# Kernel tuning notes

Measured on AMD Instinct MI355X. Metric: run time of the kernel, lower is better.

## Reference

```python
import jax, jax.numpy as jnp
import numpy as np

N_NODES = 100000
N_EDGES = 3200000
IN_CH = 128
HID_CH = 128   # 2 * out_channels
OUT_CH = 64


def setup_inputs() -> dict:
    key = jax.random.key(0)
    ks = jax.random.split(key, 6)
    x = jax.random.normal(ks[0], (N_NODES, IN_CH), dtype=jnp.float32)
    edge_index = jax.random.randint(ks[1], (2, N_EDGES), 0, N_NODES, dtype=jnp.int64)
    # Glorot-ish init for GCN linear weights
    W1 = jax.random.normal(ks[2], (IN_CH, HID_CH), dtype=jnp.float32) / np.sqrt(IN_CH)
    b1 = jnp.zeros((HID_CH,), dtype=jnp.float32)
    W2 = jax.random.normal(ks[3], (HID_CH, OUT_CH), dtype=jnp.float32) / np.sqrt(HID_CH)
    b2 = jnp.zeros((OUT_CH,), dtype=jnp.float32)
    return {"x": x, "edge_index": edge_index, "W1": W1, "b1": b1, "W2": W2, "b2": b2}


def gcn_conv(x, src, dst, W, b, n):
    """PyG GCNConv: add self-loops, symmetric D^-1/2 (A+I) D^-1/2 normalization,
    linear transform, scatter-add aggregation, then bias."""
    h = x @ W  # [N, C_out]
    ones = jnp.ones(src.shape[0], dtype=x.dtype)
    deg = jax.ops.segment_sum(ones, dst, num_segments=n) + 1.0  # self-loop degree
    dinv = jax.lax.rsqrt(deg)  # [N]
    coef = dinv[src] * dinv[dst]  # [E] edge normalization
    agg = jax.ops.segment_sum(h[src] * coef[:, None], dst, num_segments=n)
    agg = agg + h * (dinv * dinv)[:, None]  # self-loop contribution
    return agg + b


def reference(x, edge_index, W1, b1, W2, b2):
    src, dst = edge_index[0], edge_index[1]
    n = x.shape[0]
    h = jax.nn.relu(gcn_conv(x, src, dst, W1, b1, n))
    out = jax.nn.relu(gcn_conv(h, src, dst, W2, b2, n))
    return out
```

## Files before the change

kernel.cpp:

```cpp
#include <hip/hip_runtime.h>
#include <hip/hip_fp16.h>
#include <cstdint>
#include <cstddef>


#define BSHIFT 8
#define CAP    12288

typedef _Float16 half8 __attribute__((ext_vector_type(8)));
typedef float f32x4 __attribute__((ext_vector_type(4)));

__global__ __launch_bounds__(256) void k_binit(int* __restrict__ bktcur, int nbkt) {
  int b = blockIdx.x * 256 + threadIdx.x;
  if (b < nbkt) bktcur[b] = b * CAP;
}

__global__ __launch_bounds__(256) void k_part(const int* __restrict__ src,
                                              const int* __restrict__ dst,
                                              int* __restrict__ bktcur,
                                              int* __restrict__ part, int E,
                                              int nbkt) {
  __shared__ int hist[512];
  const int tid = threadIdx.x;
  const int e0 = blockIdx.x * 4096;
  for (int b = tid; b < nbkt; b += 256) hist[b] = 0;
  __syncthreads();
#pragma unroll
  for (int j = 0; j < 16; ++j) {
    const int e = e0 + j * 256 + tid;
    if (e < E) atomicAdd(&hist[dst[e] >> BSHIFT], 1);
  }
  __syncthreads();
  for (int b = tid; b < nbkt; b += 256) {
    const int c = hist[b];
    hist[b] = c ? atomicAdd(&bktcur[b], c) : 0;
  }
  __syncthreads();
#pragma unroll
  for (int j = 0; j < 16; ++j) {
    const int e = e0 + j * 256 + tid;
    if (e < E) {
      const int d = dst[e];
      const int bkt = d >> BSHIFT;
      const int pos = atomicAdd(&hist[bkt], 1);
      if (pos < (bkt + 1) * CAP)
        part[pos] = (src[e] << BSHIFT) | (d & ((1 << BSHIFT) - 1));
    }
  }
}

__global__ __launch_bounds__(256) void k_bktscan(const int* __restrict__ bktcur,
                                                 int* __restrict__ bktbase,
                                                 int* __restrict__ offsets, int n,
                                                 int E, int nbkt) {
  __shared__ int sc[512];
  const int t = threadIdx.x;
  sc[t] = (t < nbkt) ? (bktcur[t] - t * CAP) : 0;
  sc[256 + t] = (256 + t < nbkt) ? (bktcur[256 + t] - (256 + t) * CAP) : 0;
  __syncthreads();
  if (t == 0) {
    int run = 0;
    for (int b = 0; b < nbkt; ++b) {
      const int c = sc[b];
      sc[b] = run;
      run += c;
    }
    offsets[n] = E;
    bktbase[nbkt] = E;
  }
  __syncthreads();
  if (t < nbkt) bktbase[t] = sc[t];
  if (256 + t < nbkt) bktbase[256 + t] = sc[256 + t];
}

__global__ __launch_bounds__(256) void k_csr2(const int* __restrict__ part,
                                              const int* __restrict__ bktcur,
                                              const int* __restrict__ bktbase,
                                              int* __restrict__ offsets,
                                              int* __restrict__ csr_src,
                                              float* __restrict__ dinv, int n) {
  __shared__ int cnt[256];
  __shared__ int ts[256];
  const int b = blockIdx.x;
  const int node0 = b << BSHIFT;
  const int nn = min(256, n - node0);
  const int t = threadIdx.x;
  cnt[t] = 0;
  __syncthreads();
  const int w0p = b * CAP;
  const int w1p = min(bktcur[b], w0p + CAP);
  for (int e = w0p + t; e < w1p; e += 256)
    atomicAdd(&cnt[part[e] & ((1 << BSHIFT) - 1)], 1);
  __syncthreads();
  const int c = cnt[t];
  ts[t] = c;
  __syncthreads();
  for (int off = 1; off < 256; off <<= 1) {
    const int u = (t >= off) ? ts[t - off] : 0;
    __syncthreads();
    ts[t] += u;
    __syncthreads();
  }
  const int excl = ts[t] - c;
  const int w0 = bktbase[b];
  if (t < nn) {
    offsets[node0 + t] = w0 + excl;
    dinv[node0 + t] = rsqrtf((float)c + 1.0f);
  }
  cnt[t] = w0 + excl;
  __syncthreads();
  for (int e = w0p + t; e < w1p; e += 256) {
    const int p = part[e];
    const int pos = atomicAdd(&cnt[p & ((1 << BSHIFT) - 1)], 1);
    csr_src[pos] = p >> BSHIFT;
  }
}

template <typename TA, int COLS>
__global__ __launch_bounds__(256) void k_gemm_mfma(const TA* __restrict__ A,
                                                   const float* __restrict__ W,
                                                   const float* __restrict__ dinv,
                                                   __half* __restrict__ Hout,
                                                   int N, int ntiles) {
  constexpr int RW = (COLS == 128) ? 2 : 4;
  constexpr int RPT = RW * 16;
  __shared__ _Float16 Wt[128 * COLS];
  __shared__ _Float16 Lb[4][16][72];
  const int tid = threadIdx.x;
  const int w = tid >> 6;
  const int l = tid & 63;

  for (int f = tid; f < (128 * COLS) / 4; f += 256) {
    const int k = f / (COLS / 4);
    const int c4 = (f % (COLS / 4)) * 4;
    const float4 wv = *reinterpret_cast<const float4*>(W + (size_t)k * COLS + c4);
#pragma unroll
    for (int j = 0; j < 4; ++j) {
      const int cc = c4 + j;
      Wt[(cc * 128 + k) ^ ((cc & 7) << 3)] = (_Float16)(&wv.x)[j];
    }
  }
  __syncthreads();

  const int colw = (COLS == 128) ? (w >> 1) * 64 : 0;
  const int rw = (COLS == 128) ? (w & 1) : w;
  const int koff = (l >> 4) * 8;

  half8 bf[4][4];
#pragma unroll
  for (int t = 0; t < 4; ++t)
#pragma unroll
    for (int s = 0; s < 4; ++s) {
      const int cc = colw + 16 * t + (l & 15);
      const int kk = 32 * s + koff;
      bf[t][s] =
          *reinterpret_cast<const half8*>(&Wt[(cc * 128 + kk) ^ ((cc & 7) << 3)]);
    }

  for (int tile = blockIdx.x; tile < ntiles; tile += gridDim.x) {
    const int row = tile * RPT + rw * 16 + (l & 15);
    const int rowc = (row < N) ? row : (N - 1);
    f32x4 acc[4];
#pragma unroll
    for (int t = 0; t < 4; ++t) acc[t] = (f32x4){0.f, 0.f, 0.f, 0.f};

#pragma unroll
    for (int s = 0; s < 4; ++s) {
      half8 af;
      if constexpr (sizeof(TA) == 4) {
        const float* ap = (const float*)A + (size_t)rowc * 128 + 32 * s + koff;
        const float4 a0 = *reinterpret_cast<const float4*>(ap);
        const float4 a1 = *reinterpret_cast<const float4*>(ap + 4);
#pragma unroll
        for (int j = 0; j < 4; ++j) {
          af[j] = (_Float16)(&a0.x)[j];
          af[4 + j] = (_Float16)(&a1.x)[j];
        }
      } else {
        af = *reinterpret_cast<const half8*>((const __half*)A +
                                             (size_t)rowc * 128 + 32 * s + koff);
      }
#pragma unroll
      for (int t = 0; t < 4; ++t)
        acc[t] = __builtin_amdgcn_mfma_f32_16x16x32_f16(af, bf[t][s], acc[t],
                                                        0, 0, 0);
    }

    const int rbase = tile * RPT + rw * 16 + (l >> 4) * 4;
    float dr[4];
#pragma unroll
    for (int r = 0; r < 4; ++r) {
      const int rr = rbase + r;
      dr[r] = (rr < N) ? dinv[rr] : 0.f;
    }

#pragma unroll
    for (int t = 0; t < 4; ++t)
#pragma unroll
      for (int r = 0; r < 4; ++r)
        Lb[w][(l >> 4) * 4 + r][16 * t + (l & 15)] = (_Float16)(acc[t][r] * dr[r]);
    const int orow = tile * RPT + rw * 16 + (l & 15);
    if (orow < N) {
      const int ch = (l >> 4) * 16;
      const half8 v0 = *reinterpret_cast<const half8*>(&Lb[w][l & 15][ch]);
      const half8 v1 = *reinterpret_cast<const half8*>(&Lb[w][l & 15][ch + 8]);
      __half* hp = Hout + (size_t)orow * COLS + colw + ch;
      *reinterpret_cast<half8*>(hp) = v0;
      *reinterpret_cast<half8*>(hp + 8) = v1;
    }
  }
}

__global__ __launch_bounds__(256) void k_gather128(
    const __half* __restrict__ H, const int* __restrict__ offsets,
    const int* __restrict__ csr_src, const float* __restrict__ dinv,
    const float* __restrict__ bias, __half* __restrict__ out, int N) {
  const int lane = threadIdx.x & 63;
  const int g = lane >> 3;
  const int sl = lane & 7;
  int w = (blockIdx.x * 256 + threadIdx.x) >> 6;
  const int nw = (gridDim.x * 256) >> 6;
  for (int i = w; i < N; i += nw) {
    const int beg = offsets[i];
    const int end = offsets[i + 1];
    float acc[16];
    {
      const float vf = (g == 0) ? 1.f : 0.f;
      const float4 ha = *reinterpret_cast<const float4*>(H + (size_t)i * 128 + sl * 16);
      const float4 hb = *reinterpret_cast<const float4*>(H + (size_t)i * 128 + sl * 16 + 8);
      const __half2* pa = reinterpret_cast<const __half2*>(&ha);
      const __half2* pb = reinterpret_cast<const __half2*>(&hb);
#pragma unroll
      for (int q = 0; q < 4; ++q) {
        const float2 fa = __half22float2(pa[q]);
        const float2 fb = __half22float2(pb[q]);
        acc[q * 2] = vf * fa.x;
        acc[q * 2 + 1] = vf * fa.y;
        acc[8 + q * 2] = vf * fb.x;
        acc[8 + q * 2 + 1] = vf * fb.y;
      }
    }
    int base = beg;
    for (; base + 16 <= end; base += 16) {
      const int s0 = __builtin_nontemporal_load(csr_src + base + g);
      const int s1 = __builtin_nontemporal_load(csr_src + base + 8 + g);
      const float4 h0a = *reinterpret_cast<const float4*>(H + (size_t)s0 * 128 + sl * 16);
      const float4 h0b = *reinterpret_cast<const float4*>(H + (size_t)s0 * 128 + sl * 16 + 8);
      const float4 h1a = *reinterpret_cast<const float4*>(H + (size_t)s1 * 128 + sl * 16);
      const float4 h1b = *reinterpret_cast<const float4*>(H + (size_t)s1 * 128 + sl * 16 + 8);
      const __half2* p0a = reinterpret_cast<const __half2*>(&h0a);
      const __half2* p0b = reinterpret_cast<const __half2*>(&h0b);
      const __half2* p1a = reinterpret_cast<const __half2*>(&h1a);
      const __half2* p1b = reinterpret_cast<const __half2*>(&h1b);
#pragma unroll
      for (int q = 0; q < 4; ++q) {
        const float2 f0a = __half22float2(p0a[q]);
        const float2 f0b = __half22float2(p0b[q]);
        const float2 f1a = __half22float2(p1a[q]);
        const float2 f1b = __half22float2(p1b[q]);
        acc[q * 2] += f0a.x + f1a.x;
        acc[q * 2 + 1] += f0a.y + f1a.y;
        acc[8 + q * 2] += f0b.x + f1b.x;
        acc[8 + q * 2 + 1] += f0b.y + f1b.y;
      }
    }
    for (; base < end; base += 8) {
      const int e = base + g;
      const bool v = e < end;
      const int s = v ? __builtin_nontemporal_load(csr_src + e) : i;
      const float vf = v ? 1.f : 0.f;
      const float4 ha = *reinterpret_cast<const float4*>(H + (size_t)s * 128 + sl * 16);
      const float4 hb = *reinterpret_cast<const float4*>(H + (size_t)s * 128 + sl * 16 + 8);
      const __half2* pa = reinterpret_cast<const __half2*>(&ha);
      const __half2* pb = reinterpret_cast<const __half2*>(&hb);
#pragma unroll
      for (int q = 0; q < 4; ++q) {
        const float2 fa = __half22float2(pa[q]);
        const float2 fb = __half22float2(pb[q]);
        acc[q * 2] = fmaf(vf, fa.x, acc[q * 2]);
        acc[q * 2 + 1] = fmaf(vf, fa.y, acc[q * 2 + 1]);
        acc[8 + q * 2] = fmaf(vf, fb.x, acc[8 + q * 2]);
        acc[8 + q * 2 + 1] = fmaf(vf, fb.y, acc[8 + q * 2 + 1]);
      }
    }
#pragma unroll
    for (int j = 0; j < 16; ++j) {
      float a = acc[j];
      a += __shfl_xor(a, 8);
      a += __shfl_xor(a, 16);
      a += __shfl_xor(a, 32);
      acc[j] = a;
    }
    if (g == 0) {
      const float di = dinv[i];
      __half2 ov[8];
#pragma unroll
      for (int q = 0; q < 8; ++q) {
        const float2 bv = *reinterpret_cast<const float2*>(bias + sl * 16 + q * 2);
        ov[q] = __floats2half2_rn(fmaxf(fmaf(di, acc[q * 2], bv.x), 0.f),
                                  fmaxf(fmaf(di, acc[q * 2 + 1], bv.y), 0.f));
      }
      __half* op = out + (size_t)i * 128 + sl * 16;
      *reinterpret_cast<float4*>(op) = *reinterpret_cast<const float4*>(&ov[0]);
      *reinterpret_cast<float4*>(op + 8) = *reinterpret_cast<const float4*>(&ov[4]);
    }
  }
}

__global__ __launch_bounds__(256) void k_gather64(
    const __half* __restrict__ H, const int* __restrict__ offsets,
    const int* __restrict__ csr_src, const float* __restrict__ dinv,
    const float* __restrict__ bias, float* __restrict__ out, int N) {
  const int lane = threadIdx.x & 63;
  const int g = lane >> 3;
  const int sl = lane & 7;
  int w = (blockIdx.x * 256 + threadIdx.x) >> 6;
  const int nw = (gridDim.x * 256) >> 6;
  for (int i = w; i < N; i += nw) {
    const int beg = offsets[i];
    const int end = offsets[i + 1];
    float acc[8];
    {
      const float vf = (g == 0) ? 1.f : 0.f;
      const float4 ha = *reinterpret_cast<const float4*>(H + (size_t)i * 64 + sl * 8);
      const __half2* pa = reinterpret_cast<const __half2*>(&ha);
#pragma unroll
      for (int q = 0; q < 4; ++q) {
        const float2 fa = __half22float2(pa[q]);
        acc[q * 2] = vf * fa.x;
        acc[q * 2 + 1] = vf * fa.y;
      }
    }
    int base = beg;
    for (; base + 16 <= end; base += 16) {
      const int s0 = __builtin_nontemporal_load(csr_src + base + g);
      const int s1 = __builtin_nontemporal_load(csr_src + base + 8 + g);
      const float4 h0 = *reinterpret_cast<const float4*>(H + (size_t)s0 * 64 + sl * 8);
      const float4 h1 = *reinterpret_cast<const float4*>(H + (size_t)s1 * 64 + sl * 8);
      const __half2* p0 = reinterpret_cast<const __half2*>(&h0);
      const __half2* p1 = reinterpret_cast<const __half2*>(&h1);
#pragma unroll
      for (int q = 0; q < 4; ++q) {
        const float2 f0 = __half22float2(p0[q]);
        const float2 f1 = __half22float2(p1[q]);
        acc[q * 2] += f0.x + f1.x;
        acc[q * 2 + 1] += f0.y + f1.y;
      }
    }
    for (; base < end; base += 8) {
      const int e = base + g;
      const bool v = e < end;
      const int s = v ? __builtin_nontemporal_load(csr_src + e) : i;
      const float vf = v ? 1.f : 0.f;
      const float4 ha = *reinterpret_cast<const float4*>(H + (size_t)s * 64 + sl * 8);
      const __half2* pa = reinterpret_cast<const __half2*>(&ha);
#pragma unroll
      for (int q = 0; q < 4; ++q) {
        const float2 fa = __half22float2(pa[q]);
        acc[q * 2] = fmaf(vf, fa.x, acc[q * 2]);
        acc[q * 2 + 1] = fmaf(vf, fa.y, acc[q * 2 + 1]);
      }
    }
#pragma unroll
    for (int j = 0; j < 8; ++j) {
      float a = acc[j];
      a += __shfl_xor(a, 8);
      a += __shfl_xor(a, 16);
      a += __shfl_xor(a, 32);
      acc[j] = a;
    }
    if (g == 0) {
      const float di = dinv[i];
      float* op = out + (size_t)i * 64 + sl * 8;
      const float4 b0 = *reinterpret_cast<const float4*>(bias + sl * 8);
      const float4 b1 = *reinterpret_cast<const float4*>(bias + sl * 8 + 4);
      float4 o;
      o.x = fmaxf(fmaf(di, acc[0], b0.x), 0.f);
      o.y = fmaxf(fmaf(di, acc[1], b0.y), 0.f);
      o.z = fmaxf(fmaf(di, acc[2], b0.z), 0.f);
      o.w = fmaxf(fmaf(di, acc[3], b0.w), 0.f);
      *reinterpret_cast<float4*>(op) = o;
      o.x = fmaxf(fmaf(di, acc[4], b1.x), 0.f);
      o.y = fmaxf(fmaf(di, acc[5], b1.y), 0.f);
      o.z = fmaxf(fmaf(di, acc[6], b1.z), 0.f);
      o.w = fmaxf(fmaf(di, acc[7], b1.w), 0.f);
      *reinterpret_cast<float4*>(op + 4) = o;
    }
  }
}

extern "C" void kernel_launch(void* const* d_in, const int* in_sizes, int n_in,
                              void* d_out, int out_size, void* d_ws,
                              size_t ws_size, hipStream_t stream) {
  const float* x  = (const float*)d_in[0];
  const int*   ei = (const int*)d_in[1];
  const float* W1 = (const float*)d_in[2];
  const float* b1 = (const float*)d_in[3];
  const float* W2 = (const float*)d_in[4];
  const float* b2 = (const float*)d_in[5];

  const int IN  = 128;
  const int n   = in_sizes[0] / IN;
  const int E   = in_sizes[1] / 2;
  const int* srcv = ei;
  const int* dstv = ei + E;
  float* out = (float*)d_out;

  const int NBKT = (n + 255) >> BSHIFT;
  const int NCHK = (E + 4095) / 4096;
  const int NT1  = (n + 31) / 32;
  const int NT2  = (n + 63) / 64;

  char* p = (char*)d_ws;
  auto take = [&](size_t bytes) {
    char* r = p;
    p += (bytes + 255) & ~(size_t)255;
    return r;
  };
  float*  dinv    = (float*)take((size_t)n * 4);
  int*    offsets = (int*)take((size_t)(n + 1) * 4);
  int*    bktbase = (int*)take(512 * 4);
  int*    bktcur  = (int*)take(512 * 4);
  int*    csr_src = (int*)take((size_t)E * 4);
  __half* H16     = (__half*)take((size_t)n * 128 * 2);
  __half* hprime  = (__half*)take((size_t)n * 128 * 2);
  int*    part    = (int*)hprime;

  k_binit<<<(NBKT + 255) / 256, 256, 0, stream>>>(bktcur, NBKT);
  k_part<<<NCHK, 256, 0, stream>>>(srcv, dstv, bktcur, part, E, NBKT);
  k_bktscan<<<1, 256, 0, stream>>>(bktcur, bktbase, offsets, n, E, NBKT);
  k_csr2<<<NBKT, 256, 0, stream>>>(part, bktcur, bktbase, offsets, csr_src,
                                   dinv, n);

  k_gemm_mfma<float, 128><<<512, 256, 0, stream>>>(x, W1, dinv, H16, n, NT1);
  k_gather128<<<25000, 256, 0, stream>>>(H16, offsets, csr_src, dinv, b1,
                                         hprime, n);

  k_gemm_mfma<__half, 64><<<512, 256, 0, stream>>>(hprime, W2, dinv, H16, n, NT2);
  k_gather64<<<25000, 256, 0, stream>>>(H16, offsets, csr_src, dinv, b2,
                                        out, n);
}
```

Baseline: 316.0 us.

## Two-pass radix partition by source then destination; shrink gather grid

Edges are first bucketed by source node, then re-bucketed by destination in a second pass. Because the second pass is stable, each destination bucket comes out with its edges in roughly sorted source order, so later neighbor gathers read features with better locality. This adds a full extra pass over the edge list, plus a scratch buffer aliased onto H16. The gather kernels also drop from 25000 to 2048 blocks, which assumes they loop over nodes with a grid stride.

```diff
diff --git a/kernel.cpp b/kernel.cpp
--- a/kernel.cpp
+++ b/kernel.cpp
@@ -10,16 +10,20 @@
 typedef _Float16 half8 __attribute__((ext_vector_type(8)));
 typedef float f32x4 __attribute__((ext_vector_type(4)));
 
-__global__ __launch_bounds__(256) void k_binit(int* __restrict__ bktcur, int nbkt) {
+__global__ __launch_bounds__(256) void k_binit2(int* __restrict__ cur0,
+                                                int* __restrict__ cur1, int nbkt) {
   int b = blockIdx.x * 256 + threadIdx.x;
-  if (b < nbkt) bktcur[b] = b * CAP;
-}
-
-__global__ __launch_bounds__(256) void k_part(const int* __restrict__ src,
-                                              const int* __restrict__ dst,
-                                              int* __restrict__ bktcur,
-                                              int* __restrict__ part, int E,
-                                              int nbkt) {
+  if (b < nbkt) {
+    cur0[b] = b * CAP;
+    cur1[b] = b * CAP;
+  }
+}
+
+__global__ __launch_bounds__(256) void k_part0(const int* __restrict__ src,
+                                               const int* __restrict__ dst,
+                                               int* __restrict__ cur0,
+                                               int* __restrict__ part0, int E,
+                                               int nbkt) {
   __shared__ int hist[512];
   const int tid = threadIdx.x;
   const int e0 = blockIdx.x * 4096;
@@ -28,7 +32,52 @@
 #pragma unroll
   for (int j = 0; j < 16; ++j) {
     const int e = e0 + j * 256 + tid;
-    if (e < E) atomicAdd(&hist[dst[e] >> BSHIFT], 1);
+    if (e < E) atomicAdd(&hist[src[e] >> BSHIFT], 1);
+  }
+  __syncthreads();
+  for (int b = tid; b < nbkt; b += 256) {
+    const int c = hist[b];
+    hist[b] = c ? atomicAdd(&cur0[b], c) : 0;
+  }
+  __syncthreads();
+#pragma unroll
+  for (int j = 0; j < 16; ++j) {
+    const int e = e0 + j * 256 + tid;
+    if (e < E) {
+      const int s = src[e];
+      const int bkt = s >> BSHIFT;
+      const int pos = atomicAdd(&hist[bkt], 1);
+      if (pos < (bkt + 1) * CAP)
+        part0[pos] = (dst[e] << BSHIFT) | (s & ((1 << BSHIFT) - 1));
+    }
+  }
+}
+
+__global__ __launch_bounds__(256) void k_part1(const int* __restrict__ part0,
+                                               const int* __restrict__ cur0,
+                                               int* __restrict__ bktcur,
+                                               int* __restrict__ part, int nbkt) {
+  __shared__ int hist[512];
+  const int tid = threadIdx.x;
+  const int e0 = blockIdx.x * 4096;
+  for (int b = tid; b < nbkt; b += 256) hist[b] = 0;
+  __syncthreads();
+  int fv[16];
+  int db[16];
+#pragma unroll
+  for (int j = 0; j < 16; ++j) {
+    const int pos = e0 + j * 256 + tid;
+    const int sb = pos / CAP;
+    db[j] = -1;
+    fv[j] = 0;
+    if (sb < nbkt && pos < cur0[sb]) {
+      const int p = __builtin_nontemporal_load(part0 + pos);
+      const int d = p >> BSHIFT;
+      const int s = (sb << BSHIFT) | (p & ((1 << BSHIFT) - 1));
+      fv[j] = (s << BSHIFT) | (d & ((1 << BSHIFT) - 1));
+      db[j] = d >> BSHIFT;
+      atomicAdd(&hist[db[j]], 1);
+    }
   }
   __syncthreads();
   for (int b = tid; b < nbkt; b += 256) {
@@ -38,13 +87,9 @@
   __syncthreads();
 #pragma unroll
   for (int j = 0; j < 16; ++j) {
-    const int e = e0 + j * 256 + tid;
-    if (e < E) {
-      const int d = dst[e];
-      const int bkt = d >> BSHIFT;
-      const int pos = atomicAdd(&hist[bkt], 1);
-      if (pos < (bkt + 1) * CAP)
-        part[pos] = (src[e] << BSHIFT) | (d & ((1 << BSHIFT) - 1));
+    if (db[j] >= 0) {
+      const int pos = atomicAdd(&hist[db[j]], 1);
+      if (pos < (db[j] + 1) * CAP) part[pos] = fv[j];
     }
   }
 }
@@ -408,6 +453,7 @@
 
   const int NBKT = (n + 255) >> BSHIFT;
   const int NCHK = (E + 4095) / 4096;
+  const int NP1  = (NBKT * CAP + 4095) / 4096;
   const int NT1  = (n + 31) / 32;
   const int NT2  = (n + 63) / 64;
 
@@ -421,22 +467,25 @@
   int*    offsets = (int*)take((size_t)(n + 1) * 4);
   int*    bktbase = (int*)take(512 * 4);
   int*    bktcur  = (int*)take(512 * 4);
+  int*    bktcur0 = (int*)take(512 * 4);
   int*    csr_src = (int*)take((size_t)E * 4);
   __half* H16     = (__half*)take((size_t)n * 128 * 2);
   __half* hprime  = (__half*)take((size_t)n * 128 * 2);
+  int*    part0   = (int*)H16;
   int*    part    = (int*)hprime;
 
-  k_binit<<<(NBKT + 255) / 256, 256, 0, stream>>>(bktcur, NBKT);
-  k_part<<<NCHK, 256, 0, stream>>>(srcv, dstv, bktcur, part, E, NBKT);
+  k_binit2<<<(NBKT + 255) / 256, 256, 0, stream>>>(bktcur0, bktcur, NBKT);
+  k_part0<<<NCHK, 256, 0, stream>>>(srcv, dstv, bktcur0, part0, E, NBKT);
+  k_part1<<<NP1, 256, 0, stream>>>(part0, bktcur0, bktcur, part, NBKT);
   k_bktscan<<<1, 256, 0, stream>>>(bktcur, bktbase, offsets, n, E, NBKT);
   k_csr2<<<NBKT, 256, 0, stream>>>(part, bktcur, bktbase, offsets, csr_src,
                                    dinv, n);
 
   k_gemm_mfma<float, 128><<<512, 256, 0, stream>>>(x, W1, dinv, H16, n, NT1);
-  k_gather128<<<25000, 256, 0, stream>>>(H16, offsets, csr_src, dinv, b1,
-                                         hprime, n);
+  k_gather128<<<2048, 256, 0, stream>>>(H16, offsets, csr_src, dinv, b1,
+                                        hprime, n);
 
   k_gemm_mfma<__half, 64><<<512, 256, 0, stream>>>(hprime, W2, dinv, H16, n, NT2);
-  k_gather64<<<25000, 256, 0, stream>>>(H16, offsets, csr_src, dinv, b2,
-                                        out, n);
-}
+  k_gather64<<<2048, 256, 0, stream>>>(H16, offsets, csr_src, dinv, b2,
+                                       out, n);
+}
```

Measured after the change: 355.7 us. 1.13x slower.

## Split layer-1 features into two 64-column halves for cache-friendlier gathers

Applied to the files above, without the earlier changes.

Stores the first GEMM output as two separate 64-column fp16 arrays and aggregates each half with its own gather pass, reusing the 64-wide gather kernel templated on fp16/fp32 output. The second GEMM reads its input from the two halves. The intent is to halve the random-access working set per gather pass so neighbour rows hit cache more often, at the cost of reading the CSR structure twice and an extra launch.

```diff
diff --git a/kernel.cpp b/kernel.cpp
--- a/kernel.cpp
+++ b/kernel.cpp
@@ -116,14 +116,14 @@
   }
 }
 
-template <typename TA, int COLS>
-__global__ __launch_bounds__(256) void k_gemm_mfma(const TA* __restrict__ A,
-                                                   const float* __restrict__ W,
-                                                   const float* __restrict__ dinv,
-                                                   __half* __restrict__ Hout,
-                                                   int N, int ntiles) {
-  constexpr int RW = (COLS == 128) ? 2 : 4;
-  constexpr int RPT = RW * 16;
+__global__ __launch_bounds__(256) void k_gemm1(const float* __restrict__ A,
+                                               const float* __restrict__ W,
+                                               const float* __restrict__ dinv,
+                                               __half* __restrict__ Hlo,
+                                               __half* __restrict__ Hhi,
+                                               int N, int ntiles) {
+  constexpr int COLS = 128;
+  constexpr int RPT = 32;
   __shared__ _Float16 Wt[128 * COLS];
   __shared__ _Float16 Lb[4][16][72];
   const int tid = threadIdx.x;
@@ -142,8 +142,8 @@
   }
   __syncthreads();
 
-  const int colw = (COLS == 128) ? (w >> 1) * 64 : 0;
-  const int rw = (COLS == 128) ? (w & 1) : w;
+  const int colw = (w >> 1) * 64;
+  const int rw = w & 1;
   const int koff = (l >> 4) * 8;
 
   half8 bf[4][4];
@@ -167,18 +167,13 @@
 #pragma unroll
     for (int s = 0; s < 4; ++s) {
       half8 af;
-      if constexpr (sizeof(TA) == 4) {
-        const float* ap = (const float*)A + (size_t)rowc * 128 + 32 * s + koff;
-        const float4 a0 = *reinterpret_cast<const float4*>(ap);
-        const float4 a1 = *reinterpret_cast<const float4*>(ap + 4);
-#pragma unroll
-        for (int j = 0; j < 4; ++j) {
-          af[j] = (_Float16)(&a0.x)[j];
-          af[4 + j] = (_Float16)(&a1.x)[j];
-        }
-      } else {
-        af = *reinterpret_cast<const half8*>((const __half*)A +
-                                             (size_t)rowc * 128 + 32 * s + koff);
+      const float* ap = A + (size_t)rowc * 128 + 32 * s + koff;
+      const float4 a0 = *reinterpret_cast<const float4*>(ap);
+      const float4 a1 = *reinterpret_cast<const float4*>(ap + 4);
+#pragma unroll
+      for (int j = 0; j < 4; ++j) {
+        af[j] = (_Float16)(&a0.x)[j];
+        af[4 + j] = (_Float16)(&a1.x)[j];
       }
 #pragma unroll
       for (int t = 0; t < 4; ++t)
@@ -204,113 +199,103 @@
       const int ch = (l >> 4) * 16;
       const half8 v0 = *reinterpret_cast<const half8*>(&Lb[w][l & 15][ch]);
       const half8 v1 = *reinterpret_cast<const half8*>(&Lb[w][l & 15][ch + 8]);
-      __half* hp = Hout + (size_t)orow * COLS + colw + ch;
+      __half* base = (colw == 0) ? Hlo : Hhi;
+      __half* hp = base + (size_t)orow * 64 + ch;
       *reinterpret_cast<half8*>(hp) = v0;
       *reinterpret_cast<half8*>(hp + 8) = v1;
     }
   }
 }
 
-__global__ __launch_bounds__(256) void k_gather128(
+__global__ __launch_bounds__(256) void k_gemm2(const __half* __restrict__ Alo,
+                                               const __half* __restrict__ Ahi,
+                                               const float* __restrict__ W,
+                                               const float* __restrict__ dinv,
+                                               __half* __restrict__ Hout,
+                                               int N, int ntiles) {
+  constexpr int COLS = 64;
+  constexpr int RPT = 64;
+  __shared__ _Float16 Wt[128 * COLS];
+  __shared__ _Float16 Lb[4][16][72];
+  const int tid = threadIdx.x;
+  const int w = tid >> 6;
+  const int l = tid & 63;
+
+  for (int f = tid; f < (128 * COLS) / 4; f += 256) {
+    const int k = f / (COLS / 4);
+    const int c4 = (f % (COLS / 4)) * 4;
+    const float4 wv = *reinterpret_cast<const float4*>(W + (size_t)k * COLS + c4);
+#pragma unroll
+    for (int j = 0; j < 4; ++j) {
+      const int cc = c4 + j;
+      Wt[(cc * 128 + k) ^ ((cc & 7) << 3)] = (_Float16)(&wv.x)[j];
+    }
+  }
+  __syncthreads();
+
+  const int rw = w;
+  const int koff = (l >> 4) * 8;
+
+  half8 bf[4][4];
+#pragma unroll
+  for (int t = 0; t < 4; ++t)
+#pragma unroll
+    for (int s = 0; s < 4; ++s) {
+      const int cc = 16 * t + (l & 15);
+      const int kk = 32 * s + koff;
+      bf[t][s] =
+          *reinterpret_cast<const half8*>(&Wt[(cc * 128 + kk) ^ ((cc & 7) << 3)]);
+    }
+
+  for (int tile = blockIdx.x; tile < ntiles; tile += gridDim.x) {
+    const int row = tile * RPT + rw * 16 + (l & 15);
+    const int rowc = (row < N) ? row : (N - 1);
+    f32x4 acc[4];
+#pragma unroll
+    for (int t = 0; t < 4; ++t) acc[t] = (f32x4){0.f, 0.f, 0.f, 0.f};
+
+#pragma unroll
+    for (int s = 0; s < 4; ++s) {
+      const __half* ab = (s < 2) ? Alo : Ahi;
+      const int kk = (s & 1) * 32 + koff;
+      const half8 af =
+          *reinterpret_cast<const half8*>(ab + (size_t)rowc * 64 + kk);
+#pragma unroll
+      for (int t = 0; t < 4; ++t)
+        acc[t] = __builtin_amdgcn_mfma_f32_16x16x32_f16(af, bf[t][s], acc[t],
+                                                        0, 0, 0);
+    }
+
+    const int rbase = tile * RPT + rw * 16 + (l >> 4) * 4;
+    float dr[4];
+#pragma unroll
+    for (int r = 0; r < 4; ++r) {
+      const int rr = rbase + r;
+      dr[r] = (rr < N) ? dinv[rr] : 0.f;
+    }
+
+#pragma unroll
+    for (int t = 0; t < 4; ++t)
+#pragma unroll
+      for (int r = 0; r < 4; ++r)
+        Lb[w][(l >> 4) * 4 + r][16 * t + (l & 15)] = (_Float16)(acc[t][r] * dr[r]);
+    const int orow = tile * RPT + rw * 16 + (l & 15);
+    if (orow < N) {
+      const int ch = (l >> 4) * 16;
+      const half8 v0 = *reinterpret_cast<const half8*>(&Lb[w][l & 15][ch]);
+      const half8 v1 = *reinterpret_cast<const half8*>(&Lb[w][l & 15][ch + 8]);
+      __half* hp = Hout + (size_t)orow * 64 + ch;
+      *reinterpret_cast<half8*>(hp) = v0;
+      *reinterpret_cast<half8*>(hp + 8) = v1;
+    }
+  }
+}
+
+template <int OUT16>
+__global__ __launch_bounds__(256) void k_gather64t(
     const __half* __restrict__ H, const int* __restrict__ offsets,
     const int* __restrict__ csr_src, const float* __restrict__ dinv,
-    const float* __restrict__ bias, __half* __restrict__ out, int N) {
-  const int lane = threadIdx.x & 63;
-  const int g = lane >> 3;
-  const int sl = lane & 7;
-  int w = (blockIdx.x * 256 + threadIdx.x) >> 6;
-  const int nw = (gridDim.x * 256) >> 6;
-  for (int i = w; i < N; i += nw) {
-    const int beg = offsets[i];
-    const int end = offsets[i + 1];
-    float acc[16];
-    {
-      const float vf = (g == 0) ? 1.f : 0.f;
-      const float4 ha = *reinterpret_cast<const float4*>(H + (size_t)i * 128 + sl * 16);
-      const float4 hb = *reinterpret_cast<const float4*>(H + (size_t)i * 128 + sl * 16 + 8);
-      const __half2* pa = reinterpret_cast<const __half2*>(&ha);
-      const __half2* pb = reinterpret_cast<const __half2*>(&hb);
-#pragma unroll
-      for (int q = 0; q < 4; ++q) {
-        const float2 fa = __half22float2(pa[q]);
-        const float2 fb = __half22float2(pb[q]);
-        acc[q * 2] = vf * fa.x;
-        acc[q * 2 + 1] = vf * fa.y;
-        acc[8 + q * 2] = vf * fb.x;
-        acc[8 + q * 2 + 1] = vf * fb.y;
-      }
-    }
-    int base = beg;
-    for (; base + 16 <= end; base += 16) {
-      const int s0 = __builtin_nontemporal_load(csr_src + base + g);
-      const int s1 = __builtin_nontemporal_load(csr_src + base + 8 + g);
-      const float4 h0a = *reinterpret_cast<const float4*>(H + (size_t)s0 * 128 + sl * 16);
-      const float4 h0b = *reinterpret_cast<const float4*>(H + (size_t)s0 * 128 + sl * 16 + 8);
-      const float4 h1a = *reinterpret_cast<const float4*>(H + (size_t)s1 * 128 + sl * 16);
-      const float4 h1b = *reinterpret_cast<const float4*>(H + (size_t)s1 * 128 + sl * 16 + 8);
-      const __half2* p0a = reinterpret_cast<const __half2*>(&h0a);
-      const __half2* p0b = reinterpret_cast<const __half2*>(&h0b);
-      const __half2* p1a = reinterpret_cast<const __half2*>(&h1a);
-      const __half2* p1b = reinterpret_cast<const __half2*>(&h1b);
-#pragma unroll
-      for (int q = 0; q < 4; ++q) {
-        const float2 f0a = __half22float2(p0a[q]);
-        const float2 f0b = __half22float2(p0b[q]);
-        const float2 f1a = __half22float2(p1a[q]);
-        const float2 f1b = __half22float2(p1b[q]);
-        acc[q * 2] += f0a.x + f1a.x;
-        acc[q * 2 + 1] += f0a.y + f1a.y;
-        acc[8 + q * 2] += f0b.x + f1b.x;
-        acc[8 + q * 2 + 1] += f0b.y + f1b.y;
-      }
-    }
-    for (; base < end; base += 8) {
-      const int e = base + g;
-      const bool v = e < end;
-      const int s = v ? __builtin_nontemporal_load(csr_src + e) : i;
-      const float vf = v ? 1.f : 0.f;
-      const float4 ha = *reinterpret_cast<const float4*>(H + (size_t)s * 128 + sl * 16);
-      const float4 hb = *reinterpret_cast<const float4*>(H + (size_t)s * 128 + sl * 16 + 8);
-      const __half2* pa = reinterpret_cast<const __half2*>(&ha);
-      const __half2* pb = reinterpret_cast<const __half2*>(&hb);
-#pragma unroll
-      for (int q = 0; q < 4; ++q) {
-        const float2 fa = __half22float2(pa[q]);
-        const float2 fb = __half22float2(pb[q]);
-        acc[q * 2] = fmaf(vf, fa.x, acc[q * 2]);
-        acc[q * 2 + 1] = fmaf(vf, fa.y, acc[q * 2 + 1]);
-        acc[8 + q * 2] = fmaf(vf, fb.x, acc[8 + q * 2]);
-        acc[8 + q * 2 + 1] = fmaf(vf, fb.y, acc[8 + q * 2 + 1]);
-      }
-    }
-#pragma unroll
-    for (int j = 0; j < 16; ++j) {
-      float a = acc[j];
-      a += __shfl_xor(a, 8);
-      a += __shfl_xor(a, 16);
-      a += __shfl_xor(a, 32);
-      acc[j] = a;
-    }
-    if (g == 0) {
-      const float di = dinv[i];
-      __half2 ov[8];
-#pragma unroll
-      for (int q = 0; q < 8; ++q) {
-        const float2 bv = *reinterpret_cast<const float2*>(bias + sl * 16 + q * 2);
-        ov[q] = __floats2half2_rn(fmaxf(fmaf(di, acc[q * 2], bv.x), 0.f),
-                                  fmaxf(fmaf(di, acc[q * 2 + 1], bv.y), 0.f));
-      }
-      __half* op = out + (size_t)i * 128 + sl * 16;
-      *reinterpret_cast<float4*>(op) = *reinterpret_cast<const float4*>(&ov[0]);
-      *reinterpret_cast<float4*>(op + 8) = *reinterpret_cast<const float4*>(&ov[4]);
-    }
-  }
-}
-
-__global__ __launch_bounds__(256) void k_gather64(
-    const __half* __restrict__ H, const int* __restrict__ offsets,
-    const int* __restrict__ csr_src, const float* __restrict__ dinv,
-    const float* __restrict__ bias, float* __restrict__ out, int N) {
+    const float* __restrict__ bias, void* __restrict__ outv, int N) {
   const int lane = threadIdx.x & 63;
   const int g = lane >> 3;
   const int sl = lane & 7;
@@ -371,20 +356,32 @@
     }
     if (g == 0) {
       const float di = dinv[i];
-      float* op = out + (size_t)i * 64 + sl * 8;
-      const float4 b0 = *reinterpret_cast<const float4*>(bias + sl * 8);
-      const float4 b1 = *reinterpret_cast<const float4*>(bias + sl * 8 + 4);
-      float4 o;
-      o.x = fmaxf(fmaf(di, acc[0], b0.x), 0.f);
-      o.y = fmaxf(fmaf(di, acc[1], b0.y), 0.f);
-      o.z = fmaxf(fmaf(di, acc[2], b0.z), 0.f);
-      o.w = fmaxf(fmaf(di, acc[3], b0.w), 0.f);
-      *reinterpret_cast<float4*>(op) = o;
-      o.x = fmaxf(fmaf(di, acc[4], b1.x), 0.f);
-      o.y = fmaxf(fmaf(di, acc[5], b1.y), 0.f);
-      o.z = fmaxf(fmaf(di, acc[6], b1.z), 0.f);
-      o.w = fmaxf(fmaf(di, acc[7], b1.w), 0.f);
-      *reinterpret_cast<float4*>(op + 4) = o;
+      if constexpr (OUT16) {
+        __half2 ov[4];
+#pragma unroll
+        for (int q = 0; q < 4; ++q) {
+          const float2 bv = *reinterpret_cast<const float2*>(bias + sl * 8 + q * 2);
+          ov[q] = __floats2half2_rn(fmaxf(fmaf(di, acc[q * 2], bv.x), 0.f),
+                                    fmaxf(fmaf(di, acc[q * 2 + 1], bv.y), 0.f));
+        }
+        __half* op = (__half*)outv + (size_t)i * 64 + sl * 8;
+        *reinterpret_cast<float4*>(op) = *reinterpret_cast<const float4*>(&ov[0]);
+      } else {
+        float* op = (float*)outv + (size_t)i * 64 + sl * 8;
+        const float4 b0 = *reinterpret_cast<const float4*>(bias + sl * 8);
+        const float4 b1 = *reinterpret_cast<const float4*>(bias + sl * 8 + 4);
+        float4 o;
+        o.x = fmaxf(fmaf(di, acc[0], b0.x), 0.f);
+        o.y = fmaxf(fmaf(di, acc[1], b0.y), 0.f);
+        o.z = fmaxf(fmaf(di, acc[2], b0.z), 0.f);
+        o.w = fmaxf(fmaf(di, acc[3], b0.w), 0.f);
+        *reinterpret_cast<float4*>(op) = o;
+        o.x = fmaxf(fmaf(di, acc[4], b1.x), 0.f);
+        o.y = fmaxf(fmaf(di, acc[5], b1.y), 0.f);
+        o.z = fmaxf(fmaf(di, acc[6], b1.z), 0.f);
+        o.w = fmaxf(fmaf(di, acc[7], b1.w), 0.f);
+        *reinterpret_cast<float4*>(op + 4) = o;
+      }
     }
   }
 }
@@ -422,9 +419,11 @@
   int*    bktbase = (int*)take(512 * 4);
   int*    bktcur  = (int*)take(512 * 4);
   int*    csr_src = (int*)take((size_t)E * 4);
-  __half* H16     = (__half*)take((size_t)n * 128 * 2);
-  __half* hprime  = (__half*)take((size_t)n * 128 * 2);
-  int*    part    = (int*)hprime;
+  __half* Hlo     = (__half*)take((size_t)n * 64 * 2);
+  __half* Hhi     = (__half*)take((size_t)n * 64 * 2);
+  __half* hplo    = (__half*)take((size_t)n * 64 * 2);
+  __half* hphi    = (__half*)take((size_t)n * 64 * 2);
+  int*    part    = (int*)hplo;
 
   k_binit<<<(NBKT + 255) / 256, 256, 0, stream>>>(bktcur, NBKT);
   k_part<<<NCHK, 256, 0, stream>>>(srcv, dstv, bktcur, part, E, NBKT);
@@ -432,11 +431,13 @@
   k_csr2<<<NBKT, 256, 0, stream>>>(part, bktcur, bktbase, offsets, csr_src,
                                    dinv, n);
 
-  k_gemm_mfma<float, 128><<<512, 256, 0, stream>>>(x, W1, dinv, H16, n, NT1);
-  k_gather128<<<25000, 256, 0, stream>>>(H16, offsets, csr_src, dinv, b1,
-                                         hprime, n);
-
-  k_gemm_mfma<__half, 64><<<512, 256, 0, stream>>>(hprime, W2, dinv, H16, n, NT2);
-  k_gather64<<<25000, 256, 0, stream>>>(H16, offsets, csr_src, dinv, b2,
-                                        out, n);
-}
+  k_gemm1<<<512, 256, 0, stream>>>(x, W1, dinv, Hlo, Hhi, n, NT1);
+  k_gather64t<1><<<25000, 256, 0, stream>>>(Hlo, offsets, csr_src, dinv, b1,
+                                            hplo, n);
+  k_gather64t<1><<<25000, 256, 0, stream>>>(Hhi, offsets, csr_src, dinv,
+                                            b1 + 64, hphi, n);
+
+  k_gemm2<<<512, 256, 0, stream>>>(hplo, hphi, W2, dinv, Hlo, n, NT2);
+  k_gather64t<0><<<25000, 256, 0, stream>>>(Hlo, offsets, csr_src, dinv, b2,
+                                            out, n);
+}
```

New measurement: 326.1 us. +3.2%, slower.

## Stage partitioned edges in shared memory for coalesced bucket writes

Applied to the files above, without the earlier changes.

The partition kernel now keeps each edge's bucket id and packed value in registers instead of re-reading src/dst in a second pass. Each block computes local bucket offsets with a serial scan, scatters entries into a shared-memory staging array sorted by bucket, then writes them out contiguously per bucket. The goal is to turn scattered global stores into mostly coalesced runs. The cost is about 24KB of extra LDS per block, one more barrier phase, and a single-thread serial scan over up to 512 buckets.

```diff
diff --git a/kernel.cpp b/kernel.cpp
--- a/kernel.cpp
+++ b/kernel.cpp
@@ -15,37 +15,68 @@
   if (b < nbkt) bktcur[b] = b * CAP;
 }
 
-__global__ __launch_bounds__(256) void k_part(const int* __restrict__ src,
-                                              const int* __restrict__ dst,
-                                              int* __restrict__ bktcur,
-                                              int* __restrict__ part, int E,
-                                              int nbkt) {
+__global__ __launch_bounds__(256) void k_part3(const int* __restrict__ src,
+                                               const int* __restrict__ dst,
+                                               int* __restrict__ bktcur,
+                                               int* __restrict__ part, int E,
+                                               int nbkt) {
+  __shared__ int vals[4096];
+  __shared__ unsigned short bid[4096];
   __shared__ int hist[512];
+  __shared__ int lbase[512];
+  __shared__ int gbase[512];
   const int tid = threadIdx.x;
   const int e0 = blockIdx.x * 4096;
+  const int ecnt = min(4096, E - e0);
   for (int b = tid; b < nbkt; b += 256) hist[b] = 0;
   __syncthreads();
+
+  int eb[16], ev[16];
 #pragma unroll
   for (int j = 0; j < 16; ++j) {
     const int e = e0 + j * 256 + tid;
-    if (e < E) atomicAdd(&hist[dst[e] >> BSHIFT], 1);
+    eb[j] = -1;
+    ev[j] = 0;
+    if (e < E) {
+      const int d = dst[e];
+      eb[j] = d >> BSHIFT;
+      ev[j] = (src[e] << BSHIFT) | (d & ((1 << BSHIFT) - 1));
+      atomicAdd(&hist[eb[j]], 1);
+    }
+  }
+  __syncthreads();
+
+  if (tid == 0) {
+    int run = 0;
+    for (int b = 0; b < nbkt; ++b) {
+      const int c = hist[b];
+      lbase[b] = run;
+      run += c;
+    }
   }
   __syncthreads();
   for (int b = tid; b < nbkt; b += 256) {
     const int c = hist[b];
-    hist[b] = c ? atomicAdd(&bktcur[b], c) : 0;
-  }
-  __syncthreads();
+    gbase[b] = c ? atomicAdd(&bktcur[b], c) : 0;
+    hist[b] = lbase[b];
+  }
+  __syncthreads();
+
 #pragma unroll
   for (int j = 0; j < 16; ++j) {
-    const int e = e0 + j * 256 + tid;
-    if (e < E) {
-      const int d = dst[e];
-      const int bkt = d >> BSHIFT;
-      const int pos = atomicAdd(&hist[bkt], 1);
-      if (pos < (bkt + 1) * CAP)
-        part[pos] = (src[e] << BSHIFT) | (d & ((1 << BSHIFT) - 1));
-    }
+    if (eb[j] >= 0) {
+      const int lpos = atomicAdd(&hist[eb[j]], 1);
+      vals[lpos] = ev[j];
+      bid[lpos] = (unsigned short)eb[j];
+    }
+  }
+  __syncthreads();
+
+  for (int s = tid; s < ecnt; s += 256) {
+    const int b = bid[s];
+    const int gpos = gbase[b] + (s - lbase[b]);
+    if (gpos < (b + 1) * CAP)
+      part[gpos] = vals[s];
   }
 }
 
@@ -427,7 +458,7 @@
   int*    part    = (int*)hprime;
 
   k_binit<<<(NBKT + 255) / 256, 256, 0, stream>>>(bktcur, NBKT);
-  k_part<<<NCHK, 256, 0, stream>>>(srcv, dstv, bktcur, part, E, NBKT);
+  k_part3<<<NCHK, 256, 0, stream>>>(srcv, dstv, bktcur, part, E, NBKT);
   k_bktscan<<<1, 256, 0, stream>>>(bktcur, bktbase, offsets, n, E, NBKT);
   k_csr2<<<NBKT, 256, 0, stream>>>(part, bktcur, bktbase, offsets, csr_src,
                                    dinv, n);
```

Result: faster. 298.6 us (-5.5%).
